# Kernel optimization log

Measured on AMD Instinct MI355X. Metric: run time of the kernel, lower is better.

Reference implementation:

```python
import jax, jax.numpy as jnp
import numpy as np

B, L, D, N, NL = 8, 32768, 64, 16, 4


def setup_inputs() -> dict:
    key = jax.random.key(0)
    ks = jax.random.split(key, 32)
    r = lambda i, shape, s=1.0: s * jax.random.normal(ks[i], shape, dtype=jnp.float32)
    return {
        "inputs": r(0, (B, L)),
        "w_init": r(1, (D, 1), 0.5), "b_init": r(2, (D,), 0.1),
        "s4_ln_w": 1.0 + r(3, (NL, D), 0.05), "s4_ln_b": r(4, (NL, D), 0.05),
        "log_dt": r(5, (NL, D), 0.5) - 4.0,          # dt ~ exp(-4) ~ 0.018
        "log_A_real": r(6, (NL, D, N), 0.3),
        "A_imag": r(7, (NL, D, N)),
        "C_re": r(8, (NL, D, N), 0.5), "C_im": r(9, (NL, D, N), 0.5),
        "D_skip": r(10, (NL, D)),
        "s4_out_w": r(11, (NL, 2 * D, D), 0.1), "s4_out_b": r(12, (NL, 2 * D), 0.05),
        "ff_ln_w": 1.0 + r(13, (NL, D), 0.05), "ff_ln_b": r(14, (NL, D), 0.05),
        "ff_w1": r(15, (NL, 2 * D, D), 0.1), "ff_b1": r(16, (NL, 2 * D), 0.05),
        "ff_w2": r(17, (NL, D, 2 * D), 0.1), "ff_b2": r(18, (NL, D), 0.05),
        "norm_w": 1.0 + r(19, (D,), 0.05), "norm_b": r(20, (D,), 0.05),
        "w_final1": r(21, (D, D), 0.1), "b_final1": r(22, (D,), 0.05),
        "w_zero": r(23, (1, D), 0.02), "b_zero": r(24, (1,), 0.01),
    }


def _ln(x, w, b):
    # layernorm over channel dim of [B, D, L] (TransposedLN)
    m = jnp.mean(x, axis=1, keepdims=True)
    v = jnp.var(x, axis=1, keepdims=True)
    return (x - m) * jax.lax.rsqrt(v + 1e-5) * w[None, :, None] + b[None, :, None]


def _s4d(z, log_dt, log_A_real, A_imag, C_re, C_im, D_skip):
    # S4D (diagonal SSM) with ZOH discretization; z: [B, D, L]
    Lq = z.shape[-1]
    dt = jnp.exp(log_dt)                              # [D]
    A = -jnp.exp(log_A_real) + 1j * A_imag            # [D, N]
    dtA = A * dt[:, None]                             # [D, N]
    C = (C_re + 1j * C_im) * (jnp.exp(dtA) - 1.0) / A # dC = C * (e^{dtA}-1)/A
    t = jnp.arange(Lq)
    # Vandermonde kernel K[d, l] = 2 Re sum_n dC[d,n] e^{dtA[d,n] * l}
    K = 2.0 * jnp.real(jnp.einsum('dn,dnl->dl', C, jnp.exp(dtA[:, :, None] * t)))
    n = 2 * Lq
    y = jnp.fft.irfft(jnp.fft.rfft(z, n) * jnp.fft.rfft(K, n)[None], n)[..., :Lq]
    return y + D_skip[None, :, None] * z


def reference(inputs, w_init, b_init, s4_ln_w, s4_ln_b, log_dt, log_A_real,
              A_imag, C_re, C_im, D_skip, s4_out_w, s4_out_b, ff_ln_w, ff_ln_b,
              ff_w1, ff_b1, ff_w2, ff_b2, norm_w, norm_b, w_final1, b_final1,
              w_zero, b_zero):
    # init conv (1x1) + ReLU; inputs [B, L] -> x [B, D, L]
    x = jax.nn.relu(jnp.einsum('dc,bcl->bdl', w_init, inputs[:, None, :])
                    + b_init[None, :, None])
    for i in range(NL):
        # --- S4 residual block: LN -> S4D -> GELU -> 1x1 conv to 2D -> GLU ---
        z = _ln(x, s4_ln_w[i], s4_ln_b[i])
        y = _s4d(z, log_dt[i], log_A_real[i], A_imag[i], C_re[i], C_im[i], D_skip[i])
        y = jax.nn.gelu(y)
        u = jnp.einsum('ed,bdl->bel', s4_out_w[i], y) + s4_out_b[i][None, :, None]
        a, g = jnp.split(u, 2, axis=1)
        x = x + a * jax.nn.sigmoid(g)
        z = _ln(x, ff_ln_w[i], ff_ln_b[i])
        h = jax.nn.gelu(jnp.einsum('ed,bdl->bel', ff_w1[i], z) + ff_b1[i][None, :, None])
        x = x + jnp.einsum('de,bel->bdl', ff_w2[i], h) + ff_b2[i][None, :, None]
    # final norm + conv head
    x = _ln(x, norm_w, norm_b)
    x = jax.nn.relu(jnp.einsum('ed,bdl->bel', w_final1, x) + b_final1[None, :, None])
    x = jnp.einsum('od,bdl->bol', w_zero, x) + b_zero[None, :, None]
    return x[:, 0, :]  # squeeze out_channels=1 -> [B, L]
```

## Files before the change

kernel.cpp:

```cpp
#include <hip/hip_runtime.h>
#include <cmath>

constexpr int Bq = 8, Lq = 32768, Dq = 64, Nq = 16, NLq = 4;
constexpr int CLq = 128, NCq = 256;
constexpr int PT = Bq * Lq / 16;

typedef _Float16 f16;
typedef _Float16 half2t __attribute__((ext_vector_type(2)));
typedef _Float16 half4 __attribute__((ext_vector_type(4)));
typedef _Float16 half8 __attribute__((ext_vector_type(8)));
typedef float f32x4 __attribute__((ext_vector_type(4)));
typedef float f32x2 __attribute__((ext_vector_type(2)));

static __device__ __forceinline__ float sigm(float x) { return 1.0f / (1.0f + __expf(-x)); }
static __device__ __forceinline__ float gelu_t(float x) {
  return x * sigm(1.5957691216057308f * fmaf(0.044715f * x * x, x, x));
}

__global__ __launch_bounds__(256) void k_setup(
    const float* __restrict__ log_dt, const float* __restrict__ log_A_real,
    const float* __restrict__ A_imag, const float* __restrict__ C_re,
    const float* __restrict__ C_im,
    f32x2* __restrict__ LAM, f32x2* __restrict__ DC2, f32x2* __restrict__ LCL) {
  int idx = blockIdx.x * 256 + threadIdx.x;
  if (idx >= NLq * Dq * Nq) return;
  int di = idx / Nq;
  float dt = expf(log_dt[di]);
  float Ar = -expf(log_A_real[idx]);
  float Ai = A_imag[idx];
  float dr = Ar * dt, dmi = Ai * dt;
  float er = expf(dr);
  float lr = er * cosf(dmi), li = er * sinf(dmi);
  float inv = 1.0f / (Ar * Ar + Ai * Ai);
  float e1r = lr - 1.0f, e1i = li;
  float qr = (e1r * Ar + e1i * Ai) * inv;
  float qi = (e1i * Ar - e1r * Ai) * inv;
  float cr = C_re[idx], ci = C_im[idx];
  LAM[idx] = f32x2{lr, li};
  DC2[idx] = f32x2{2.0f * (cr * qr - ci * qi), 2.0f * (cr * qi + ci * qr)};
  float erc = expf(dr * (float)CLq);
  LCL[idx] = f32x2{erc * cosf(dmi * (float)CLq), erc * sinf(dmi * (float)CLq)};
}

__global__ __launch_bounds__(128) void k_wtall(
    const f32x2* __restrict__ LAM, const f32x2* __restrict__ DC2,
    const f32x2* __restrict__ LCL, const float* __restrict__ dskip,
    half8* __restrict__ TF, half8* __restrict__ VF, half8* __restrict__ WF) {
  __shared__ f32x2 pw[129][16];
  __shared__ float Ks[128];
  int d = blockIdx.x & 63, L = blockIdx.x >> 6;
  const f32x2* LAMl = LAM + L * 1024;
  const f32x2* DC2l = DC2 + L * 1024;
  const f32x2* LCLl = LCL + L * 1024;
  half8* TFl = TF + (size_t)L * 131072;
  half8* VFl = VF + (size_t)L * 32768;
  half8* WFl = WF + (size_t)L * 32768;
  int t = threadIdx.x;
#pragma unroll
  for (int n = 0; n < 16; n++) {
    f32x2 lam = LAMl[d * 16 + n];
    float pr = 1.f, pi = 0.f, br = lam.x, bi = lam.y;
    int e = t;
    while (e) {
      if (e & 1) { float tt = pr * br - pi * bi; pi = fmaf(pr, bi, pi * br); pr = tt; }
      float t2 = br * br - bi * bi; bi = 2.f * br * bi; br = t2; e >>= 1;
    }
    pw[t][n] = f32x2{pr, pi};
  }
  if (t < 16) pw[128][t] = LCLl[d * 16 + t];
  __syncthreads();
  {
    float k = 0.f;
#pragma unroll
    for (int n = 0; n < 16; n++) {
      f32x2 dc = DC2l[d * 16 + n];
      f32x2 p = pw[t][n];
      k += dc.x * p.x - dc.y * p.y;
    }
    if (t == 0) k += dskip[L * 64 + d];
    Ks[t] = k;
  }
  __syncthreads();
  for (int s = t; s < 2048; s += 128) {
    int ln = s & 63, kt = (s >> 6) & 3, mt = s >> 8;
    int jo = mt * 16 + (ln & 15);
    int ji0 = kt * 32 + (ln >> 4) * 8;
    half8 v;
#pragma unroll
    for (int jj = 0; jj < 8; jj++) {
      int ji = ji0 + jj;
      v[jj] = (jo >= ji) ? (f16)Ks[jo - ji] : (f16)0.f;
    }
    TFl[(size_t)d * 2048 + s] = v;
  }
  for (int s = t; s < 512; s += 128) {
    int ln = s & 63, mt = s >> 6;
    int jo = mt * 16 + (ln & 15);
    int q0 = (ln >> 4) * 8;
    half8 v;
#pragma unroll
    for (int jj = 0; jj < 8; jj++) {
      int q = q0 + jj, n = q >> 1;
      f32x2 dc = DC2l[d * 16 + n];
      f32x2 p = pw[jo + 1][n];
      float wr = dc.x * p.x - dc.y * p.y;
      float wi = dc.x * p.y + dc.y * p.x;
      v[jj] = (q & 1) ? (f16)(-wi) : (f16)wr;
    }
    VFl[(size_t)d * 512 + s] = v;
  }
  for (int s = t; s < 512; s += 128) {
    int ln = s & 63, kt = (s >> 6) & 3, nt = s >> 8;
    int p_ = nt * 16 + (ln & 15);
    int n = p_ >> 1;
    int j0 = kt * 32 + (ln >> 4) * 8;
    half8 v;
#pragma unroll
    for (int jj = 0; jj < 8; jj++) {
      f32x2 p = pw[127 - (j0 + jj)][n];
      v[jj] = (p_ & 1) ? (f16)p.y : (f16)p.x;
    }
    WFl[(size_t)d * 512 + s] = v;
  }
}

__global__ __launch_bounds__(512) void k_init3(
    const float* __restrict__ inp, const float* __restrict__ w_init,
    const float* __restrict__ b_init, const float* __restrict__ lnw,
    const float* __restrict__ lnb, float* __restrict__ X, f16* __restrict__ Z16) {
  __shared__ __align__(16) f16 ztile[64 * 132];
  int tid = threadIdx.x;
  int widx = tid >> 6, lane = tid & 63;
  int pl = lane & 15, qh = lane >> 4;
  for (int k = 0; k < 4; ++k) {
    int pt = blockIdx.x * 8 + widx + k * 4096;
    int pos = pt * 16 + pl;
    float v = inp[pos];
    float s = 0.f, s2 = 0.f;
    f32x4 o[4];
#pragma unroll
    for (int q = 0; q < 4; q++) {
      int d0 = q * 16 + qh * 4;
      f32x4 w4 = *(const f32x4*)(w_init + d0);
      f32x4 b4 = *(const f32x4*)(b_init + d0);
#pragma unroll
      for (int j = 0; j < 4; j++) {
        float t = fmaf(w4[j], v, b4[j]);
        t = t > 0.f ? t : 0.f;
        o[q][j] = t; s += t; s2 += t * t;
      }
      *(f32x4*)(X + (size_t)pos * 64 + d0) = o[q];
    }
    s += __shfl_xor(s, 16); s += __shfl_xor(s, 32);
    s2 += __shfl_xor(s2, 16); s2 += __shfl_xor(s2, 32);
    float m = s * (1.0f / 64.0f);
    float rstd = rsqrtf(s2 * (1.0f / 64.0f) - m * m + 1e-5f);
    int prow = widx * 16 + pl;
#pragma unroll
    for (int q = 0; q < 4; q++) {
      int d0 = q * 16 + qh * 4;
      f32x4 lw = *(const f32x4*)(lnw + d0);
      f32x4 lb = *(const f32x4*)(lnb + d0);
#pragma unroll
      for (int r = 0; r < 4; r++)
        ztile[(d0 + r) * 132 + prow] = (f16)fmaf((o[q][r] - m) * rstd, lw[r], lb[r]);
    }
    __syncthreads();
    {
      int d = tid >> 3, c0 = (tid & 7) * 16;
      half8 z0 = *(const half8*)(ztile + d * 132 + c0);
      half8 z1 = *(const half8*)(ztile + d * 132 + c0 + 8);
      size_t zoff = (size_t)d * 262144 + (size_t)(blockIdx.x * 8 + k * 4096) * 16;
      *(half8*)(Z16 + zoff + c0) = z0;
      *(half8*)(Z16 + zoff + c0 + 8) = z1;
    }
    __syncthreads();
  }
}

__global__ __launch_bounds__(256) void k_p1g(
    const f16* __restrict__ Z16, const half8* __restrict__ WF, f16* __restrict__ S16) {
  int tid = threadIdx.x;
  int lane = tid & 63;
  int task = blockIdx.x * 4 + (tid >> 6);
  int d = task >> 7, bct = task & 127;
  int bc0 = bct * 16;
  int pl = lane & 15, qh = lane >> 4;
  half8 az[4];
  const f16* zp = Z16 + ((size_t)d * 2048 + bc0 + pl) * 128 + qh * 8;
#pragma unroll
  for (int kt = 0; kt < 4; kt++) az[kt] = *(const half8*)(zp + kt * 32);
#pragma unroll
  for (int nt = 0; nt < 2; nt++) {
    f32x4 acc = f32x4{0.f, 0.f, 0.f, 0.f};
#pragma unroll
    for (int kt = 0; kt < 4; kt++)
      acc = __builtin_amdgcn_mfma_f32_16x16x32_f16(az[kt], WF[(size_t)d * 512 + (nt * 4 + kt) * 64 + lane], acc, 0, 0, 0);
#pragma unroll
    for (int r = 0; r < 4; r++)
      S16[((size_t)d * 2048 + bc0 + qh * 4 + r) * 32 + nt * 16 + pl] = (f16)acc[r];
  }
}

__global__ __launch_bounds__(128) void k_pass2(
    const f16* __restrict__ S16, const f32x2* __restrict__ LCLl, f16* __restrict__ Sc) {
  int d = blockIdx.x;
  int t = threadIdx.x;
  int n = t & 15, b = t >> 4;
  f32x2 lam = LCLl[d * 16 + n];
  float cr = 0.f, ci = 0.f;
  size_t base = ((size_t)d * 2048 + b * 256) * 32 + 2 * n;
  const f16* sp = S16 + base;
  f16* cp = Sc + base;
#pragma unroll 8
  for (int c = 0; c < 256; c++) {
    *(half2t*)(cp + (size_t)c * 32) = half2t{(f16)cr, (f16)ci};
    half2t v = *(const half2t*)(sp + (size_t)c * 32);
    float nr = fmaf(lam.x, cr, fmaf(-lam.y, ci, (float)v[0]));
    float ni = fmaf(lam.x, ci, fmaf(lam.y, cr, (float)v[1]));
    cr = nr; ci = ni;
  }
}

__global__ __launch_bounds__(256) void k_p3g2(
    const f16* __restrict__ Z16, const f16* __restrict__ Sc,
    const half8* __restrict__ TF, const half8* __restrict__ VF,
    f16* __restrict__ Y16) {
  int tid = threadIdx.x;
  int lane = tid & 63, widx = tid >> 6;
  int bct = blockIdx.x & 127, dg = blockIdx.x >> 7;
  int bc0 = bct * 16;
  int dbase = dg * 16 + widx * 4;
  int pl = lane & 15, qh = lane >> 4;
  half8 zb[4][4];
  half8 sb[4];
#pragma unroll
  for (int di = 0; di < 4; di++) {
    int d = dbase + di;
    const f16* zp = Z16 + ((size_t)d * 2048 + bc0 + pl) * 128 + qh * 8;
#pragma unroll
    for (int kt = 0; kt < 4; kt++) zb[di][kt] = *(const half8*)(zp + kt * 32);
    sb[di] = *(const half8*)(Sc + ((size_t)d * 2048 + bc0 + pl) * 32 + qh * 8);
  }
#pragma unroll
  for (int mt = 0; mt < 8; mt++) {
    const int KTM = mt / 2 + 1;
    f32x4 acc[4];
#pragma unroll
    for (int di = 0; di < 4; di++) {
      int d = dbase + di;
      acc[di] = f32x4{0.f, 0.f, 0.f, 0.f};
      const half8* tfp = TF + ((size_t)d * 8 + mt) * 256 + lane;
#pragma unroll
      for (int kt = 0; kt < KTM; kt++)
        acc[di] = __builtin_amdgcn_mfma_f32_16x16x32_f16(tfp[kt * 64], zb[di][kt], acc[di], 0, 0, 0);
      acc[di] = __builtin_amdgcn_mfma_f32_16x16x32_f16(VF[((size_t)d * 8 + mt) * 64 + lane], sb[di], acc[di], 0, 0, 0);
    }
#pragma unroll
    for (int r = 0; r < 4; r++) {
      int pos = (bc0 + pl) * 128 + mt * 16 + qh * 4 + r;
      half4 pk = half4{(f16)gelu_t(acc[0][r]), (f16)gelu_t(acc[1][r]),
                       (f16)gelu_t(acc[2][r]), (f16)gelu_t(acc[3][r])};
      *(half4*)(Y16 + (size_t)pos * 64 + dbase) = pk;
    }
  }
}

template <int WZ>
__global__ __launch_bounds__(512) void k_gluff3(
    const f16* __restrict__ Y16, const float* __restrict__ Wg, const float* __restrict__ bg,
    const float* __restrict__ W1, const float* __restrict__ b1,
    const float* __restrict__ W2, const float* __restrict__ b2,
    const float* __restrict__ lnw, const float* __restrict__ lnb,
    const float* __restrict__ nlnw, const float* __restrict__ nlnb,
    float* __restrict__ X, f32x2* __restrict__ STATS, f16* __restrict__ Z16) {
  __shared__ __align__(16) char smem[68352];
  int tid = threadIdx.x;
#pragma unroll
  for (int it = 0; it < 2; it++) {
    int s = it * 512 + tid;
    int l = s & 63, ks = (s >> 6) & 1, et = s >> 7;
    const float* wp = Wg + (et * 16 + (l & 15)) * 64 + ks * 32 + (l >> 4) * 8;
    f32x4 w0 = *(const f32x4*)wp, w1 = *(const f32x4*)(wp + 4);
    *(half8*)(smem + s * 16) = half8{(f16)w0[0], (f16)w0[1], (f16)w0[2], (f16)w0[3],
                                     (f16)w1[0], (f16)w1[1], (f16)w1[2], (f16)w1[3]};
  }
#pragma unroll
  for (int it = 0; it < 2; it++) {
    int s = it * 512 + tid;
    int l = s & 63, ks = (s >> 6) & 1, et = s >> 7;
    int pl = l & 15, qh = l >> 4;
    const float* wp = W1 + (et * 16 + pl) * 64 + ks * 32 + qh * 4;
    f32x4 w0 = *(const f32x4*)wp;
    f32x4 w1 = *(const f32x4*)(wp + 16);
    *(half8*)(smem + 16384 + s * 16) = half8{(f16)w0[0], (f16)w0[1], (f16)w0[2], (f16)w0[3],
                                             (f16)w1[0], (f16)w1[1], (f16)w1[2], (f16)w1[3]};
  }
#pragma unroll
  for (int it = 0; it < 2; it++) {
    int s = it * 512 + tid;
    int l = s & 63, ks = (s >> 6) & 3, dt = s >> 8;
    int pl = l & 15, qh = l >> 4;
    const float* wp = W2 + (dt * 16 + pl) * 128 + ks * 32 + qh * 4;
    f32x4 w0 = *(const f32x4*)wp;
    f32x4 w1 = *(const f32x4*)(wp + 16);
    *(half8*)(smem + 32768 + s * 16) = half8{(f16)w0[0], (f16)w0[1], (f16)w0[2], (f16)w0[3],
                                             (f16)w1[0], (f16)w1[1], (f16)w1[2], (f16)w1[3]};
  }
  for (int idx = tid; idx < 576; idx += 512) {
    float v;
    if (idx < 128) v = bg[idx];
    else if (idx < 256) v = b1[idx - 128];
    else if (idx < 320) v = b2[idx - 256];
    else if (idx < 384) v = lnw[idx - 320];
    else if (idx < 448) v = lnb[idx - 384];
    else if (idx < 512) v = nlnw[idx - 448];
    else v = nlnb[idx - 512];
    ((float*)(smem + 49152))[idx] = v;
  }
  __syncthreads();
  int lane = tid & 63, pl = lane & 15, qh = lane >> 4;
  int widx = tid >> 6;
  f16* ztile = (f16*)(smem + 51456);

  for (int k = 0; k < 4; ++k) {
    int pt = blockIdx.x * 8 + widx + k * 4096;
    int pos = pt * 16 + pl;
    half8 yb0 = *(const half8*)(Y16 + (size_t)pos * 64 + qh * 8);
    half8 yb1 = *(const half8*)(Y16 + (size_t)pos * 64 + 32 + qh * 8);
    f32x4 xv[4];
#pragma unroll
    for (int q = 0; q < 4; q++) xv[q] = *(const f32x4*)(X + (size_t)pos * 64 + q * 16 + qh * 4);

    unsigned sb = 0;
    asm volatile("" : "+v"(sb));
    const char* sm = smem + sb;
    const half8* sWg = (const half8*)sm;
    const half8* sW1 = (const half8*)(sm + 16384);
    const half8* sW2 = (const half8*)(sm + 32768);
    const float* sf = (const float*)(sm + 49152);
    f32x4 accg[8];
#pragma unroll
    for (int et = 0; et < 8; et++) accg[et] = *(const f32x4*)(sf + et * 16 + qh * 4);
#pragma unroll
    for (int et = 0; et < 8; et++)
      accg[et] = __builtin_amdgcn_mfma_f32_16x16x32_f16(sWg[(et * 2) * 64 + lane], yb0, accg[et], 0, 0, 0);
#pragma unroll
    for (int et = 0; et < 8; et++)
      accg[et] = __builtin_amdgcn_mfma_f32_16x16x32_f16(sWg[(et * 2 + 1) * 64 + lane], yb1, accg[et], 0, 0, 0);
    float s = 0.f, s2 = 0.f;
#pragma unroll
    for (int q = 0; q < 4; q++)
#pragma unroll
      for (int r = 0; r < 4; r++) {
        xv[q][r] += accg[q][r] * sigm(accg[q + 4][r]);
        s += xv[q][r]; s2 += xv[q][r] * xv[q][r];
      }
    s += __shfl_xor(s, 16); s += __shfl_xor(s, 32);
    s2 += __shfl_xor(s2, 16); s2 += __shfl_xor(s2, 32);
    float m = s * (1.0f / 64.0f);
    float rstd = rsqrtf(s2 * (1.0f / 64.0f) - m * m + 1e-5f);
    half4 zb4[4];
#pragma unroll
    for (int ks = 0; ks < 4; ks++) {
      f32x4 lw = *(const f32x4*)(sf + 320 + ks * 16 + qh * 4);
      f32x4 lb = *(const f32x4*)(sf + 384 + ks * 16 + qh * 4);
      half4 z;
#pragma unroll
      for (int r = 0; r < 4; r++) z[r] = (f16)fmaf((xv[ks][r] - m) * rstd, lw[r], lb[r]);
      zb4[ks] = z;
    }
    f32x4 acc1[8];
#pragma unroll
    for (int et = 0; et < 8; et++) acc1[et] = *(const f32x4*)(sf + 128 + et * 16 + qh * 4);
#pragma unroll
    for (int ks = 0; ks < 2; ks++) {
      half4 a = zb4[ks * 2], b = zb4[ks * 2 + 1];
      half8 zb8 = half8{a[0], a[1], a[2], a[3], b[0], b[1], b[2], b[3]};
#pragma unroll
      for (int et = 0; et < 8; et++)
        acc1[et] = __builtin_amdgcn_mfma_f32_16x16x32_f16(sW1[(et * 2 + ks) * 64 + lane], zb8, acc1[et], 0, 0, 0);
    }
    half4 h4[8];
#pragma unroll
    for (int et = 0; et < 8; et++)
      h4[et] = half4{(f16)gelu_t(acc1[et][0]), (f16)gelu_t(acc1[et][1]),
                     (f16)gelu_t(acc1[et][2]), (f16)gelu_t(acc1[et][3])};
    f32x4 acc2[4];
#pragma unroll
    for (int dt = 0; dt < 4; dt++) acc2[dt] = *(const f32x4*)(sf + 256 + dt * 16 + qh * 4);
#pragma unroll
    for (int ks = 0; ks < 4; ks++) {
      half4 a = h4[ks * 2], b = h4[ks * 2 + 1];
      half8 hb8 = half8{a[0], a[1], a[2], a[3], b[0], b[1], b[2], b[3]};
#pragma unroll
      for (int dt = 0; dt < 4; dt++)
        acc2[dt] = __builtin_amdgcn_mfma_f32_16x16x32_f16(sW2[(dt * 4 + ks) * 64 + lane], hb8, acc2[dt], 0, 0, 0);
    }
    s = 0.f; s2 = 0.f;
#pragma unroll
    for (int dt = 0; dt < 4; dt++) {
#pragma unroll
      for (int r = 0; r < 4; r++) {
        xv[dt][r] += acc2[dt][r];
        s += xv[dt][r]; s2 += xv[dt][r] * xv[dt][r];
      }
      *(f32x4*)(X + (size_t)pos * 64 + dt * 16 + qh * 4) = xv[dt];
    }
    s += __shfl_xor(s, 16); s += __shfl_xor(s, 32);
    s2 += __shfl_xor(s2, 16); s2 += __shfl_xor(s2, 32);
    float m2 = s * (1.0f / 64.0f);
    float rstd2 = rsqrtf(s2 * (1.0f / 64.0f) - m2 * m2 + 1e-5f);

    if constexpr (WZ) {
      int prow = widx * 16 + pl;
#pragma unroll
      for (int q = 0; q < 4; q++) {
        int d0 = q * 16 + qh * 4;
        f32x4 lw = *(const f32x4*)(sf + 448 + d0);
        f32x4 lb = *(const f32x4*)(sf + 512 + d0);
#pragma unroll
        for (int r = 0; r < 4; r++)
          ztile[(d0 + r) * 132 + prow] = (f16)fmaf((xv[q][r] - m2) * rstd2, lw[r], lb[r]);
      }
      __syncthreads();
      {
        int d = tid >> 3, c0 = (tid & 7) * 16;
        half8 z0 = *(const half8*)(ztile + d * 132 + c0);
        half8 z1 = *(const half8*)(ztile + d * 132 + c0 + 8);
        size_t zoff = (size_t)d * 262144 + (size_t)(blockIdx.x * 8 + k * 4096) * 16;
        *(half8*)(Z16 + zoff + c0) = z0;
        *(half8*)(Z16 + zoff + c0 + 8) = z1;
      }
      __syncthreads();
    } else {
      if (qh == 0) STATS[pos] = f32x2{m2, rstd2};
    }
  }
}

__global__ __launch_bounds__(256) void k_head(
    const float* __restrict__ X, const f32x2* __restrict__ STATS,
    const float* __restrict__ nw_, const float* __restrict__ nb_,
    const float* __restrict__ Wf, const float* __restrict__ bfb,
    const float* __restrict__ wz, const float* __restrict__ bz,
    float* __restrict__ outp) {
  int lane = threadIdx.x & 63;
  int wv = (blockIdx.x * 256 + threadIdx.x) >> 6;
  int nwv = gridDim.x * 4;
  int pl = lane & 15, qh = lane >> 4;
  half4 af[4][4];
#pragma unroll
  for (int et = 0; et < 4; et++)
#pragma unroll
    for (int ks = 0; ks < 4; ks++) {
      f32x4 w4 = *(const f32x4*)(Wf + (et * 16 + pl) * 64 + ks * 16 + qh * 4);
      af[et][ks] = half4{(f16)w4[0], (f16)w4[1], (f16)w4[2], (f16)w4[3]};
    }
  float bz0 = bz[0];
  for (int pt = wv; pt < PT; pt += nwv) {
    int pos = pt * 16 + pl;
    f32x2 ms = STATS[pos];
    half4 bf[4];
#pragma unroll
    for (int ks = 0; ks < 4; ks++) {
      f32x4 x4 = *(const f32x4*)(X + (size_t)pos * 64 + ks * 16 + qh * 4);
      f32x4 lw = *(const f32x4*)(nw_ + ks * 16 + qh * 4);
      f32x4 lb = *(const f32x4*)(nb_ + ks * 16 + qh * 4);
      f32x4 z;
#pragma unroll
      for (int j = 0; j < 4; j++) z[j] = fmaf((x4[j] - ms.x) * ms.y, lw[j], lb[j]);
      bf[ks] = half4{(f16)z[0], (f16)z[1], (f16)z[2], (f16)z[3]};
    }
    f32x4 acc[4];
#pragma unroll
    for (int et = 0; et < 4; et++) acc[et] = *(const f32x4*)(bfb + et * 16 + qh * 4);
#pragma unroll
    for (int ks = 0; ks < 4; ks++)
#pragma unroll
      for (int et = 0; et < 4; et++)
        acc[et] = __builtin_amdgcn_mfma_f32_16x16x16f16(af[et][ks], bf[ks], acc[et], 0, 0, 0);
    float o = 0.f;
#pragma unroll
    for (int et = 0; et < 4; et++) {
      f32x4 wzv = *(const f32x4*)(wz + et * 16 + qh * 4);
#pragma unroll
      for (int r = 0; r < 4; r++) {
        float rv = acc[et][r];
        rv = rv > 0.f ? rv : 0.f;
        o = fmaf(wzv[r], rv, o);
      }
    }
    o += __shfl_xor(o, 16); o += __shfl_xor(o, 32);
    if (qh == 0) outp[pos] = o + bz0;
  }
}

extern "C" void kernel_launch(void* const* d_in, const int* in_sizes, int n_in,
                              void* d_out, int out_size, void* d_ws, size_t ws_size,
                              hipStream_t stream) {
  (void)in_sizes; (void)n_in; (void)out_size; (void)ws_size;
  const float* inputs   = (const float*)d_in[0];
  const float* w_init   = (const float*)d_in[1];
  const float* b_init   = (const float*)d_in[2];
  const float* s4_ln_w  = (const float*)d_in[3];
  const float* s4_ln_b  = (const float*)d_in[4];
  const float* log_dt   = (const float*)d_in[5];
  const float* log_A    = (const float*)d_in[6];
  const float* A_imag   = (const float*)d_in[7];
  const float* C_re     = (const float*)d_in[8];
  const float* C_im     = (const float*)d_in[9];
  const float* D_skip   = (const float*)d_in[10];
  const float* s4_out_w = (const float*)d_in[11];
  const float* s4_out_b = (const float*)d_in[12];
  const float* ff_ln_w  = (const float*)d_in[13];
  const float* ff_ln_b  = (const float*)d_in[14];
  const float* ff_w1    = (const float*)d_in[15];
  const float* ff_b1    = (const float*)d_in[16];
  const float* ff_w2    = (const float*)d_in[17];
  const float* ff_b2    = (const float*)d_in[18];
  const float* norm_w   = (const float*)d_in[19];
  const float* norm_b   = (const float*)d_in[20];
  const float* w_final1 = (const float*)d_in[21];
  const float* b_final1 = (const float*)d_in[22];
  const float* w_zero   = (const float*)d_in[23];
  const float* b_zero   = (const float*)d_in[24];

  char* w8 = (char*)d_ws;
  size_t off = 0;
  float* X     = (float*)(w8 + off); off += (size_t)67108864;
  f16*   Z16   = (f16*)(w8 + off);   off += (size_t)33554432;
  f16*   Y16   = (f16*)(w8 + off);   off += (size_t)33554432;
  f16*   S16   = (f16*)(w8 + off);   off += (size_t)8388608;
  f16*   Sc    = (f16*)(w8 + off);   off += (size_t)8388608;
  f32x2* STATS = (f32x2*)(w8 + off); off += (size_t)2097152;
  f32x2* LAM   = (f32x2*)(w8 + off); off += 32768;
  f32x2* DC2   = (f32x2*)(w8 + off); off += 32768;
  f32x2* LCL   = (f32x2*)(w8 + off); off += 32768;
  half8* TF    = (half8*)(w8 + off); off += (size_t)8388608;
  half8* VF    = (half8*)(w8 + off); off += (size_t)2097152;
  half8* WF    = (half8*)(w8 + off); off += (size_t)2097152;

  k_setup<<<16, 256, 0, stream>>>(log_dt, log_A, A_imag, C_re, C_im, LAM, DC2, LCL);
  k_wtall<<<256, 128, 0, stream>>>(LAM, DC2, LCL, D_skip, TF, VF, WF);
  k_init3<<<512, 512, 0, stream>>>(inputs, w_init, b_init, s4_ln_w, s4_ln_b, X, Z16);
  for (int i = 0; i < NLq; i++) {
    k_p1g<<<2048, 256, 0, stream>>>(Z16, WF + (size_t)i * 32768, S16);
    k_pass2<<<64, 128, 0, stream>>>(S16, LCL + i * 1024, Sc);
    k_p3g2<<<512, 256, 0, stream>>>(Z16, Sc, TF + (size_t)i * 131072, VF + (size_t)i * 32768, Y16);
    if (i < NLq - 1) {
      k_gluff3<1><<<512, 512, 0, stream>>>(Y16, s4_out_w + i * 8192, s4_out_b + i * 128,
                                           ff_w1 + i * 8192, ff_b1 + i * 128,
                                           ff_w2 + i * 8192, ff_b2 + i * 64,
                                           ff_ln_w + i * 64, ff_ln_b + i * 64,
                                           s4_ln_w + (i + 1) * 64, s4_ln_b + (i + 1) * 64,
                                           X, STATS, Z16);
    } else {
      k_gluff3<0><<<512, 512, 0, stream>>>(Y16, s4_out_w + i * 8192, s4_out_b + i * 128,
                                           ff_w1 + i * 8192, ff_b1 + i * 128,
                                           ff_w2 + i * 8192, ff_b2 + i * 64,
                                           ff_ln_w + i * 64, ff_ln_b + i * 64,
                                           s4_ln_w, s4_ln_b,
                                           X, STATS, Z16);
    }
  }
  k_head<<<2048, 256, 0, stream>>>(X, STATS, norm_w, norm_b, w_final1, b_final1,
                                   w_zero, b_zero, (float*)d_out);
}
```

Baseline: 534.0 us.

## Fuse head into last GLU/FF kernel, merge setup into wtall, prefetch next tile

Folds the final layernorm, conv head and output projection into the last k_gluff3 instance. This removes the k_head launch, the STATS buffer and the final X write and re-read. It also merges the SSM parameter setup kernel into k_wtall, computing lambda and dC in shared memory, which saves one launch. Inside k_gluff3, the loads for the next position tile are issued ahead of the current compute, so memory latency can overlap with work. The cost is higher register pressure and shared-memory reuse of the ztile region for head weights.

Result: no change. 532.2 us (-0.3%).

```diff
diff --git a/kernel.cpp b/kernel.cpp
--- a/kernel.cpp
+++ b/kernel.cpp
@@ -17,48 +17,45 @@
   return x * sigm(1.5957691216057308f * fmaf(0.044715f * x * x, x, x));
 }
 
-__global__ __launch_bounds__(256) void k_setup(
+__global__ __launch_bounds__(128) void k_wtall(
     const float* __restrict__ log_dt, const float* __restrict__ log_A_real,
     const float* __restrict__ A_imag, const float* __restrict__ C_re,
-    const float* __restrict__ C_im,
-    f32x2* __restrict__ LAM, f32x2* __restrict__ DC2, f32x2* __restrict__ LCL) {
-  int idx = blockIdx.x * 256 + threadIdx.x;
-  if (idx >= NLq * Dq * Nq) return;
-  int di = idx / Nq;
-  float dt = expf(log_dt[di]);
-  float Ar = -expf(log_A_real[idx]);
-  float Ai = A_imag[idx];
-  float dr = Ar * dt, dmi = Ai * dt;
-  float er = expf(dr);
-  float lr = er * cosf(dmi), li = er * sinf(dmi);
-  float inv = 1.0f / (Ar * Ar + Ai * Ai);
-  float e1r = lr - 1.0f, e1i = li;
-  float qr = (e1r * Ar + e1i * Ai) * inv;
-  float qi = (e1i * Ar - e1r * Ai) * inv;
-  float cr = C_re[idx], ci = C_im[idx];
-  LAM[idx] = f32x2{lr, li};
-  DC2[idx] = f32x2{2.0f * (cr * qr - ci * qi), 2.0f * (cr * qi + ci * qr)};
-  float erc = expf(dr * (float)CLq);
-  LCL[idx] = f32x2{erc * cosf(dmi * (float)CLq), erc * sinf(dmi * (float)CLq)};
-}
-
-__global__ __launch_bounds__(128) void k_wtall(
-    const f32x2* __restrict__ LAM, const f32x2* __restrict__ DC2,
-    const f32x2* __restrict__ LCL, const float* __restrict__ dskip,
-    half8* __restrict__ TF, half8* __restrict__ VF, half8* __restrict__ WF) {
+    const float* __restrict__ C_im, const float* __restrict__ dskip,
+    f32x2* __restrict__ LCL, half8* __restrict__ TF, half8* __restrict__ VF,
+    half8* __restrict__ WF) {
   __shared__ f32x2 pw[129][16];
+  __shared__ f32x2 lamS[16], dcS[16];
   __shared__ float Ks[128];
   int d = blockIdx.x & 63, L = blockIdx.x >> 6;
-  const f32x2* LAMl = LAM + L * 1024;
-  const f32x2* DC2l = DC2 + L * 1024;
-  const f32x2* LCLl = LCL + L * 1024;
   half8* TFl = TF + (size_t)L * 131072;
   half8* VFl = VF + (size_t)L * 32768;
   half8* WFl = WF + (size_t)L * 32768;
   int t = threadIdx.x;
+  if (t < 16) {
+    int di = L * 64 + d;
+    int idx = di * 16 + t;
+    float dt = expf(log_dt[di]);
+    float Ar = -expf(log_A_real[idx]);
+    float Ai = A_imag[idx];
+    float dr = Ar * dt, dmi = Ai * dt;
+    float er = expf(dr);
+    float lr = er * cosf(dmi), li = er * sinf(dmi);
+    float inv = 1.0f / (Ar * Ar + Ai * Ai);
+    float e1r = lr - 1.0f, e1i = li;
+    float qr = (e1r * Ar + e1i * Ai) * inv;
+    float qi = (e1i * Ar - e1r * Ai) * inv;
+    float cr = C_re[idx], ci = C_im[idx];
+    lamS[t] = f32x2{lr, li};
+    dcS[t] = f32x2{2.0f * (cr * qr - ci * qi), 2.0f * (cr * qi + ci * qr)};
+    float erc = expf(dr * 128.0f);
+    f32x2 l128 = f32x2{erc * cosf(dmi * 128.0f), erc * sinf(dmi * 128.0f)};
+    pw[128][t] = l128;
+    LCL[(size_t)L * 1024 + d * 16 + t] = l128;
+  }
+  __syncthreads();
 #pragma unroll
   for (int n = 0; n < 16; n++) {
-    f32x2 lam = LAMl[d * 16 + n];
+    f32x2 lam = lamS[n];
     float pr = 1.f, pi = 0.f, br = lam.x, bi = lam.y;
     int e = t;
     while (e) {
@@ -67,13 +64,12 @@
     }
     pw[t][n] = f32x2{pr, pi};
   }
-  if (t < 16) pw[128][t] = LCLl[d * 16 + t];
   __syncthreads();
   {
     float k = 0.f;
 #pragma unroll
     for (int n = 0; n < 16; n++) {
-      f32x2 dc = DC2l[d * 16 + n];
+      f32x2 dc = dcS[n];
       f32x2 p = pw[t][n];
       k += dc.x * p.x - dc.y * p.y;
     }
@@ -101,7 +97,7 @@
 #pragma unroll
     for (int jj = 0; jj < 8; jj++) {
       int q = q0 + jj, n = q >> 1;
-      f32x2 dc = DC2l[d * 16 + n];
+      f32x2 dc = dcS[n];
       f32x2 p = pw[jo + 1][n];
       float wr = dc.x * p.x - dc.y * p.y;
       float wi = dc.x * p.y + dc.y * p.x;
@@ -273,7 +269,10 @@
     const float* __restrict__ W2, const float* __restrict__ b2,
     const float* __restrict__ lnw, const float* __restrict__ lnb,
     const float* __restrict__ nlnw, const float* __restrict__ nlnb,
-    float* __restrict__ X, f32x2* __restrict__ STATS, f16* __restrict__ Z16) {
+    float* __restrict__ X, f16* __restrict__ Z16,
+    const float* __restrict__ Wf, const float* __restrict__ bfb,
+    const float* __restrict__ wz, const float* __restrict__ bz,
+    float* __restrict__ outp) {
   __shared__ __align__(16) char smem[68352];
   int tid = threadIdx.x;
 #pragma unroll
@@ -289,8 +288,8 @@
   for (int it = 0; it < 2; it++) {
     int s = it * 512 + tid;
     int l = s & 63, ks = (s >> 6) & 1, et = s >> 7;
-    int pl = l & 15, qh = l >> 4;
-    const float* wp = W1 + (et * 16 + pl) * 64 + ks * 32 + qh * 4;
+    int pls = l & 15, qhs = l >> 4;
+    const float* wp = W1 + (et * 16 + pls) * 64 + ks * 32 + qhs * 4;
     f32x4 w0 = *(const f32x4*)wp;
     f32x4 w1 = *(const f32x4*)(wp + 16);
     *(half8*)(smem + 16384 + s * 16) = half8{(f16)w0[0], (f16)w0[1], (f16)w0[2], (f16)w0[3],
@@ -300,8 +299,8 @@
   for (int it = 0; it < 2; it++) {
     int s = it * 512 + tid;
     int l = s & 63, ks = (s >> 6) & 3, dt = s >> 8;
-    int pl = l & 15, qh = l >> 4;
-    const float* wp = W2 + (dt * 16 + pl) * 128 + ks * 32 + qh * 4;
+    int pls = l & 15, qhs = l >> 4;
+    const float* wp = W2 + (dt * 16 + pls) * 128 + ks * 32 + qhs * 4;
     f32x4 w0 = *(const f32x4*)wp;
     f32x4 w1 = *(const f32x4*)(wp + 16);
     *(half8*)(smem + 32768 + s * 16) = half8{(f16)w0[0], (f16)w0[1], (f16)w0[2], (f16)w0[3],
@@ -318,19 +317,44 @@
     else v = nlnb[idx - 512];
     ((float*)(smem + 49152))[idx] = v;
   }
+  if constexpr (!WZ) {
+    if (tid < 512) {
+      int s = tid;
+      int l = s & 63, ks = (s >> 6) & 1, et = s >> 7;
+      int pls = l & 15, qhs = l >> 4;
+      const float* wp = Wf + (et * 16 + pls) * 64 + ks * 32 + qhs * 4;
+      f32x4 w0 = *(const f32x4*)wp;
+      f32x4 w1 = *(const f32x4*)(wp + 16);
+      *(half8*)(smem + 51456 + s * 16) = half8{(f16)w0[0], (f16)w0[1], (f16)w0[2], (f16)w0[3],
+                                               (f16)w1[0], (f16)w1[1], (f16)w1[2], (f16)w1[3]};
+    }
+    if (tid < 129) {
+      float v = tid < 64 ? bfb[tid] : (tid < 128 ? wz[tid - 64] : bz[0]);
+      ((float*)(smem + 59648))[tid] = v;
+    }
+  }
   __syncthreads();
   int lane = tid & 63, pl = lane & 15, qh = lane >> 4;
   int widx = tid >> 6;
   f16* ztile = (f16*)(smem + 51456);
 
+  int pos = (blockIdx.x * 8 + widx) * 16 + pl;
+  half8 yb0 = *(const half8*)(Y16 + (size_t)pos * 64 + qh * 8);
+  half8 yb1 = *(const half8*)(Y16 + (size_t)pos * 64 + 32 + qh * 8);
+  f32x4 xv[4];
+#pragma unroll
+  for (int q = 0; q < 4; q++) xv[q] = *(const f32x4*)(X + (size_t)pos * 64 + q * 16 + qh * 4);
+
   for (int k = 0; k < 4; ++k) {
-    int pt = blockIdx.x * 8 + widx + k * 4096;
-    int pos = pt * 16 + pl;
-    half8 yb0 = *(const half8*)(Y16 + (size_t)pos * 64 + qh * 8);
-    half8 yb1 = *(const half8*)(Y16 + (size_t)pos * 64 + 32 + qh * 8);
-    f32x4 xv[4];
-#pragma unroll
-    for (int q = 0; q < 4; q++) xv[q] = *(const f32x4*)(X + (size_t)pos * 64 + q * 16 + qh * 4);
+    half8 nyb0{}, nyb1{};
+    f32x4 nxv[4] = {};
+    int npos = pos + 65536;
+    if (k < 3) {
+      nyb0 = *(const half8*)(Y16 + (size_t)npos * 64 + qh * 8);
+      nyb1 = *(const half8*)(Y16 + (size_t)npos * 64 + 32 + qh * 8);
+#pragma unroll
+      for (int q = 0; q < 4; q++) nxv[q] = *(const f32x4*)(X + (size_t)npos * 64 + q * 16 + qh * 4);
+    }
 
     unsigned sb = 0;
     asm volatile("" : "+v"(sb));
@@ -405,7 +429,7 @@
         xv[dt][r] += acc2[dt][r];
         s += xv[dt][r]; s2 += xv[dt][r] * xv[dt][r];
       }
-      *(f32x4*)(X + (size_t)pos * 64 + dt * 16 + qh * 4) = xv[dt];
+      if constexpr (WZ) *(f32x4*)(X + (size_t)pos * 64 + dt * 16 + qh * 4) = xv[dt];
     }
     s += __shfl_xor(s, 16); s += __shfl_xor(s, 32);
     s2 += __shfl_xor(s2, 16); s2 += __shfl_xor(s2, 32);
@@ -434,65 +458,50 @@
       }
       __syncthreads();
     } else {
-      if (qh == 0) STATS[pos] = f32x2{m2, rstd2};
-    }
-  }
-}
-
-__global__ __launch_bounds__(256) void k_head(
-    const float* __restrict__ X, const f32x2* __restrict__ STATS,
-    const float* __restrict__ nw_, const float* __restrict__ nb_,
-    const float* __restrict__ Wf, const float* __restrict__ bfb,
-    const float* __restrict__ wz, const float* __restrict__ bz,
-    float* __restrict__ outp) {
-  int lane = threadIdx.x & 63;
-  int wv = (blockIdx.x * 256 + threadIdx.x) >> 6;
-  int nwv = gridDim.x * 4;
-  int pl = lane & 15, qh = lane >> 4;
-  half4 af[4][4];
-#pragma unroll
-  for (int et = 0; et < 4; et++)
-#pragma unroll
-    for (int ks = 0; ks < 4; ks++) {
-      f32x4 w4 = *(const f32x4*)(Wf + (et * 16 + pl) * 64 + ks * 16 + qh * 4);
-      af[et][ks] = half4{(f16)w4[0], (f16)w4[1], (f16)w4[2], (f16)w4[3]};
-    }
-  float bz0 = bz[0];
-  for (int pt = wv; pt < PT; pt += nwv) {
-    int pos = pt * 16 + pl;
-    f32x2 ms = STATS[pos];
-    half4 bf[4];
-#pragma unroll
-    for (int ks = 0; ks < 4; ks++) {
-      f32x4 x4 = *(const f32x4*)(X + (size_t)pos * 64 + ks * 16 + qh * 4);
-      f32x4 lw = *(const f32x4*)(nw_ + ks * 16 + qh * 4);
-      f32x4 lb = *(const f32x4*)(nb_ + ks * 16 + qh * 4);
-      f32x4 z;
-#pragma unroll
-      for (int j = 0; j < 4; j++) z[j] = fmaf((x4[j] - ms.x) * ms.y, lw[j], lb[j]);
-      bf[ks] = half4{(f16)z[0], (f16)z[1], (f16)z[2], (f16)z[3]};
-    }
-    f32x4 acc[4];
-#pragma unroll
-    for (int et = 0; et < 4; et++) acc[et] = *(const f32x4*)(bfb + et * 16 + qh * 4);
-#pragma unroll
-    for (int ks = 0; ks < 4; ks++)
-#pragma unroll
-      for (int et = 0; et < 4; et++)
-        acc[et] = __builtin_amdgcn_mfma_f32_16x16x16f16(af[et][ks], bf[ks], acc[et], 0, 0, 0);
-    float o = 0.f;
-#pragma unroll
-    for (int et = 0; et < 4; et++) {
-      f32x4 wzv = *(const f32x4*)(wz + et * 16 + qh * 4);
-#pragma unroll
-      for (int r = 0; r < 4; r++) {
-        float rv = acc[et][r];
-        rv = rv > 0.f ? rv : 0.f;
-        o = fmaf(wzv[r], rv, o);
-      }
-    }
-    o += __shfl_xor(o, 16); o += __shfl_xor(o, 32);
-    if (qh == 0) outp[pos] = o + bz0;
+      const half8* sWf = (const half8*)(sm + 51456);
+      const float* hf = (const float*)(sm + 59648);
+      half4 hz[4];
+#pragma unroll
+      for (int ks = 0; ks < 4; ks++) {
+        f32x4 lw = *(const f32x4*)(sf + 448 + ks * 16 + qh * 4);
+        f32x4 lb = *(const f32x4*)(sf + 512 + ks * 16 + qh * 4);
+        half4 z;
+#pragma unroll
+        for (int r = 0; r < 4; r++) z[r] = (f16)fmaf((xv[ks][r] - m2) * rstd2, lw[r], lb[r]);
+        hz[ks] = z;
+      }
+      f32x4 acch[4];
+#pragma unroll
+      for (int et = 0; et < 4; et++) acch[et] = *(const f32x4*)(hf + et * 16 + qh * 4);
+#pragma unroll
+      for (int ks = 0; ks < 2; ks++) {
+        half4 a = hz[ks * 2], b = hz[ks * 2 + 1];
+        half8 zb8 = half8{a[0], a[1], a[2], a[3], b[0], b[1], b[2], b[3]};
+#pragma unroll
+        for (int et = 0; et < 4; et++)
+          acch[et] = __builtin_amdgcn_mfma_f32_16x16x32_f16(sWf[(et * 2 + ks) * 64 + lane], zb8, acch[et], 0, 0, 0);
+      }
+      float o = 0.f;
+#pragma unroll
+      for (int et = 0; et < 4; et++) {
+        f32x4 wzv = *(const f32x4*)(hf + 64 + et * 16 + qh * 4);
+#pragma unroll
+        for (int r = 0; r < 4; r++) {
+          float rv = acch[et][r];
+          rv = rv > 0.f ? rv : 0.f;
+          o = fmaf(wzv[r], rv, o);
+        }
+      }
+      o += __shfl_xor(o, 16); o += __shfl_xor(o, 32);
+      if (qh == 0) outp[pos] = o + hf[128];
+    }
+
+    if (k < 3) {
+      yb0 = nyb0; yb1 = nyb1;
+#pragma unroll
+      for (int q = 0; q < 4; q++) xv[q] = nxv[q];
+      pos = npos;
+    }
   }
 }
 
@@ -533,16 +542,13 @@
   f16*   Y16   = (f16*)(w8 + off);   off += (size_t)33554432;
   f16*   S16   = (f16*)(w8 + off);   off += (size_t)8388608;
   f16*   Sc    = (f16*)(w8 + off);   off += (size_t)8388608;
-  f32x2* STATS = (f32x2*)(w8 + off); off += (size_t)2097152;
-  f32x2* LAM   = (f32x2*)(w8 + off); off += 32768;
-  f32x2* DC2   = (f32x2*)(w8 + off); off += 32768;
   f32x2* LCL   = (f32x2*)(w8 + off); off += 32768;
   half8* TF    = (half8*)(w8 + off); off += (size_t)8388608;
   half8* VF    = (half8*)(w8 + off); off += (size_t)2097152;
   half8* WF    = (half8*)(w8 + off); off += (size_t)2097152;
 
-  k_setup<<<16, 256, 0, stream>>>(log_dt, log_A, A_imag, C_re, C_im, LAM, DC2, LCL);
-  k_wtall<<<256, 128, 0, stream>>>(LAM, DC2, LCL, D_skip, TF, VF, WF);
+  k_wtall<<<256, 128, 0, stream>>>(log_dt, log_A, A_imag, C_re, C_im, D_skip,
+                                   LCL, TF, VF, WF);
   k_init3<<<512, 512, 0, stream>>>(inputs, w_init, b_init, s4_ln_w, s4_ln_b, X, Z16);
   for (int i = 0; i < NLq; i++) {
     k_p1g<<<2048, 256, 0, stream>>>(Z16, WF + (size_t)i * 32768, S16);
@@ -554,16 +560,15 @@
                                            ff_w2 + i * 8192, ff_b2 + i * 64,
                                            ff_ln_w + i * 64, ff_ln_b + i * 64,
                                            s4_ln_w + (i + 1) * 64, s4_ln_b + (i + 1) * 64,
-                                           X, STATS, Z16);
+                                           X, Z16, nullptr, nullptr, nullptr, nullptr, nullptr);
     } else {
       k_gluff3<0><<<512, 512, 0, stream>>>(Y16, s4_out_w + i * 8192, s4_out_b + i * 128,
                                            ff_w1 + i * 8192, ff_b1 + i * 128,
                                            ff_w2 + i * 8192, ff_b2 + i * 64,
                                            ff_ln_w + i * 64, ff_ln_b + i * 64,
-                                           s4_ln_w, s4_ln_b,
-                                           X, STATS, Z16);
-    }
-  }
-  k_head<<<2048, 256, 0, stream>>>(X, STATS, norm_w, norm_b, w_final1, b_final1,
-                                   w_zero, b_zero, (float*)d_out);
-}
+                                           norm_w, norm_b,
+                                           X, Z16, w_final1, b_final1, w_zero, b_zero,
+                                           (float*)d_out);
+    }
+  }
+}
```
